# Optimization experiments

Measured on AMD Instinct MI355X. Metric: run time of the kernel, lower is better.

## Reference

```python
import jax, jax.numpy as jnp
import numpy as np

N = 50000      # nodes
E = 800000     # edges
D = 128        # input_dim = nb_hidden = emb_dim
A = 4          # nb_edge_types (edge attr dim)
H = 2          # heads (MyGATConv default)
G = 128        # number of graphs (g.batch)
NEG = 0.2      # leaky_relu negative slope
L = 3          # nb_layers


def _glorot(key, shape):
    lim = np.sqrt(6.0 / (shape[-2] + shape[-1]))
    return jax.random.uniform(key, shape, minval=-lim, maxval=lim, dtype=jnp.float32)


def setup_inputs():
    key = jax.random.key(0)
    ks = jax.random.split(key, 20)
    inp = {
        "x": jax.random.normal(ks[0], (N, D), jnp.float32),
        "edge_index": jax.random.randint(ks[1], (2, E), 0, N, dtype=jnp.int32),
        "edge_attr": jax.random.normal(ks[2], (E, A), jnp.float32),
        "batch": jnp.sort(jax.random.randint(ks[3], (N,), 0, G, dtype=jnp.int32)),
    }
    for l in range(L):
        inp[f"linN{l}"] = _glorot(ks[4 + 4 * l], (D, H * D))
        inp[f"linE{l}"] = _glorot(ks[5 + 4 * l], (A, H * A))
        inp[f"att{l}"] = _glorot(ks[6 + 4 * l], (1, H, 2 * D + A))
        inp[f"bias{l}"] = jnp.zeros((H * D,), jnp.float32)
    inp["fw"] = _glorot(ks[16], (D, 1))
    inp["fb"] = jnp.zeros((1,), jnp.float32)
    return inp


def _gat_layer(x_in, e_in, src, dst, linN, linE, att, bias):
    n = x_in.shape[0]
    x = (x_in @ linN + bias).reshape(n, H, D)              # [N,H,D]
    e = (e_in @ linE).reshape(-1, H, A)                    # [E,H,A]
    # alpha = (cat([x_i, x_j, e], -1) * att).sum(-1); x_i = x[src], x_j = x[dst]
    ai = jnp.einsum('nhc,hc->nh', x, att[0, :, :D])        # per-node, gathered at src
    aj = jnp.einsum('nhc,hc->nh', x, att[0, :, D:2 * D])   # per-node, gathered at dst
    ae = jnp.einsum('ehc,hc->eh', e, att[0, :, 2 * D:])
    alpha = jax.nn.leaky_relu(ai[src] + aj[dst] + ae, NEG)  # [E,H]
    # segment softmax over targets (edge_index[1])
    amax = jax.ops.segment_max(alpha, dst, num_segments=n)
    ex = jnp.exp(alpha - amax[dst])
    denom = jax.ops.segment_sum(ex, dst, num_segments=n)
    alpha = ex / denom[dst]
    # PyG propagate: message = alpha * x[src], scatter-add at dst
    msg = alpha[:, :, None] * x[src]                       # [E,H,D]
    out = jax.ops.segment_sum(msg, dst, num_segments=n) + x
    # concat=False -> mean over heads, then ReLU
    return jax.nn.relu(out.mean(axis=1)), jax.nn.relu(e.mean(axis=1))


def reference(x, edge_index, edge_attr, batch,
              linN0, linE0, att0, bias0,
              linN1, linE1, att1, bias1,
              linN2, linE2, att2, bias2,
              fw, fb):
    src, dst = edge_index[0], edge_index[1]
    params = [(linN0, linE0, att0, bias0),
              (linN1, linE1, att1, bias1),
              (linN2, linE2, att2, bias2)]
    h, e = x, edge_attr
    for (lN, lE, at, b) in params:
        h, e = _gat_layer(h, e, src, dst, lN, lE, at, b)
    pooled = jax.ops.segment_sum(h, batch, num_segments=G)  # global_add_pool -> [G,D]
    y = (pooled @ fw + fb).squeeze(-1)                      # [G]
    return y
```

## Files before the change

### kernel.cpp

```cpp
#include <hip/hip_runtime.h>
#include <hip/hip_bf16.h>

#define DD 128
#define AA 4
#define HH 2

typedef short short8 __attribute__((ext_vector_type(8)));
typedef float f32x4 __attribute__((ext_vector_type(4)));

__device__ inline unsigned short f2bf(float f) {
    unsigned u = __float_as_uint(f);
    unsigned r = (u + 0x7fffu + ((u >> 16) & 1u)) >> 16;
    return (unsigned short)r;
}
__device__ inline float4 unpack_bf16x4(uint2 v) {
    float4 r;
    r.x = __uint_as_float(v.x << 16);
    r.y = __uint_as_float(v.x & 0xffff0000u);
    r.z = __uint_as_float(v.y << 16);
    r.w = __uint_as_float(v.y & 0xffff0000u);
    return r;
}
__device__ inline uint2 pack_bf16x4(float a, float b, float c, float d) {
    uint2 p;
    p.x = (unsigned)f2bf(a) | ((unsigned)f2bf(b) << 16);
    p.y = (unsigned)f2bf(c) | ((unsigned)f2bf(d) << 16);
    return p;
}


__global__ void rank_kernel(const int* __restrict__ dst, int* __restrict__ cnt,
                            int* __restrict__ rank, int E) {
    int e = blockIdx.x * blockDim.x + threadIdx.x;
    if (e < E) rank[e] = atomicAdd(&cnt[dst[e]], 1);
}

__global__ __launch_bounds__(256) void scan1(const int* __restrict__ cnt,
                                             int* __restrict__ bsum, int N,
                                             float* __restrict__ y,
                                             const float* __restrict__ fb) {
    __shared__ int wsh[4];
    int b = blockIdx.x, t = threadIdx.x;
    int lane = t & 63, w = t >> 6;
    if (b == 0 && t < 128) y[t] = fb[0];
    int base = b * 1024;
    int v = 0;
    #pragma unroll
    for (int i = 0; i < 4; ++i) {
        int idx = base + i * 256 + t;
        v += (idx < N) ? cnt[idx] : 0;
    }
    #pragma unroll
    for (int o = 32; o; o >>= 1) v += __shfl_xor(v, o);
    if (lane == 0) wsh[w] = v;
    __syncthreads();
    if (t == 0) bsum[b] = wsh[0] + wsh[1] + wsh[2] + wsh[3];
}

__global__ __launch_bounds__(64) void scan2(int* __restrict__ bsum, int NB,
                                            int* __restrict__ total) {
    int t = threadIdx.x;
    int v = (t < NB) ? bsum[t] : 0;
    int x = v;
    #pragma unroll
    for (int o = 1; o < 64; o <<= 1) {
        int u = __shfl_up(x, o);
        if (t >= o) x += u;
    }
    if (t < NB) bsum[t] = x - v;
    if (t == 63) *total = x;
}

__global__ __launch_bounds__(256) void scan3(const int* __restrict__ cnt,
                                             const int* __restrict__ bsum,
                                             int* __restrict__ row_off, int N) {
    __shared__ int wtot[4];
    __shared__ int carry;
    int b = blockIdx.x, t = threadIdx.x;
    int lane = t & 63, w = t >> 6;
    if (t == 0) carry = bsum[b];
    __syncthreads();
    int base = b * 1024;
    #pragma unroll
    for (int it = 0; it < 4; ++it) {
        int idx = base + it * 256 + t;
        int v = (idx < N) ? cnt[idx] : 0;
        int x = v;
        #pragma unroll
        for (int o = 1; o < 64; o <<= 1) {
            int u = __shfl_up(x, o);
            if (lane >= o) x += u;
        }
        if (lane == 63) wtot[w] = x;
        __syncthreads();
        int woff = 0;
        for (int i = 0; i < w; ++i) woff += wtot[i];
        int c = carry;
        __syncthreads();
        if (t == 255) carry = c + woff + x;
        int ex = c + woff + x - v;
        if (idx < N) row_off[idx] = ex;
        __syncthreads();
    }
}

__global__ void perm_kernel(const int* __restrict__ dst, const int* __restrict__ rank,
                            const int* __restrict__ row_off, int* __restrict__ perm, int E) {
    int e = blockIdx.x * blockDim.x + threadIdx.x;
    if (e >= E) return;
    perm[row_off[dst[e]] + rank[e]] = e;
}


__device__ inline void edge_stage(const float4& ev, const float* __restrict__ linE,
                                  const float* __restrict__ att, float2& ae, float4& enext) {
    float eh[8];
    #pragma unroll
    for (int c = 0; c < 8; ++c)
        eh[c] = ev.x * linE[c] + ev.y * linE[8 + c] + ev.z * linE[16 + c] + ev.w * linE[24 + c];
    float a0 = 0.f, a1 = 0.f;
    #pragma unroll
    for (int a = 0; a < 4; ++a) {
        a0 += eh[a]     * att[2 * DD + a];
        a1 += eh[4 + a] * att[(2 * DD + AA) + 2 * DD + a];
    }
    ae.x = a0; ae.y = a1;
    enext.x = fmaxf(0.5f * (eh[0] + eh[4]), 0.f);
    enext.y = fmaxf(0.5f * (eh[1] + eh[5]), 0.f);
    enext.z = fmaxf(0.5f * (eh[2] + eh[6]), 0.f);
    enext.w = fmaxf(0.5f * (eh[3] + eh[7]), 0.f);
}

__global__ __launch_bounds__(256) void prep_fused(
        const float* __restrict__ ein, const int* __restrict__ src,
        const int* __restrict__ perm,
        const float* __restrict__ linE0, const float* __restrict__ att0,
        const float* __restrict__ linE1, const float* __restrict__ att1,
        const float* __restrict__ linE2, const float* __restrict__ att2,
        int* __restrict__ csr_src,
        float2* __restrict__ ae0, float2* __restrict__ ae1, float2* __restrict__ ae2,
        int E, int ebE,
        const float* __restrict__ X, uint2* __restrict__ As, int N, int ebA,
        const float* __restrict__ W0, const float* __restrict__ W1,
        const float* __restrict__ W2, unsigned short* __restrict__ Bs) {
    int b = blockIdx.x;
    if (b < ebE) {
        int p = b * 256 + threadIdx.x;
        if (p >= E) return;
        int e = perm[p];
        csr_src[p] = src[e];
        float4 ev = ((const float4*)ein)[e];
        float2 ae; float4 en;
        edge_stage(ev, linE0, att0, ae, en); ae0[p] = ae;
        edge_stage(en, linE1, att1, ae, ev); ae1[p] = ae;
        edge_stage(ev, linE2, att2, ae, en); ae2[p] = ae;
    } else if (b < ebE + ebA) {
        int t = (b - ebE) * 256 + threadIdx.x;
        if (t >= N * 32) return;
        int r = t >> 5, kq4 = t & 31;
        float4 v = ((const float4*)X)[t];
        int g = r >> 4, m = r & 15;
        int ks = kq4 >> 3, q = (kq4 >> 1) & 3;
        int cell = ((g * 4 + ks) * 4 + q) * 16 + m;
        As[cell * 2 + (kq4 & 1)] = pack_bf16x4(v.x, v.y, v.z, v.w);
    } else {
        int t = (b - ebE - ebA) * 256 + threadIdx.x;
        if (t >= 3 * 128 * 64) return;
        int l = t / (128 * 64);
        int r = t - l * (128 * 64);
        const float* W = (l == 0) ? W0 : (l == 1) ? W1 : W2;
        unsigned short* B = Bs + (size_t)l * 128 * 256;
        int k = r >> 6, c4g = r & 63;
        float4 v = ((const float4*)W)[r];
        int ct = c4g >> 2, n0 = (c4g & 3) * 4;
        int ks = k >> 5, q = (k >> 3) & 3, j = k & 7;
        int cellbase = ((ct * 4 + ks) * 4 + q) * 16 + n0;
        B[(cellbase + 0) * 8 + j] = f2bf(v.x);
        B[(cellbase + 1) * 8 + j] = f2bf(v.y);
        B[(cellbase + 2) * 8 + j] = f2bf(v.z);
        B[(cellbase + 3) * 8 + j] = f2bf(v.w);
    }
}


__global__ __launch_bounds__(256) void gemm_mfma(const short8* __restrict__ As,
                                                 const short8* __restrict__ Bs,
                                                 const float* __restrict__ bias,
                                                 const float* __restrict__ att,
                                                 uint2* __restrict__ xhb,
                                                 float* __restrict__ aiaj, int Ngroups) {
    __shared__ __align__(16) unsigned short sh[4][16 * 132];
    int w = threadIdx.x >> 6;
    int flat = blockIdx.x * 4 + w;
    int wid = flat >> 1, half = flat & 1;
    int lane = threadIdx.x & 63;
    if (wid >= Ngroups) return;
    int q = lane >> 4, m = lane & 15;

    const short8* Ag = As + (size_t)wid * 256;
    f32x4 acc[8];
    #pragma unroll
    for (int c8 = 0; c8 < 8; ++c8) acc[c8] = (f32x4){0.f, 0.f, 0.f, 0.f};

    #pragma unroll
    for (int ks = 0; ks < 4; ++ks) {
        short8 a = Ag[ks * 64 + lane];
        #pragma unroll
        for (int c8 = 0; c8 < 8; ++c8) {
            short8 b = Bs[(half * 8 + c8) * 256 + ks * 64 + lane];
            acc[c8] = __builtin_amdgcn_mfma_f32_16x16x32_bf16(a, b, acc[c8], 0, 0, 0);
        }
    }

    const float* atth = att + half * (2 * DD + AA);
    float ai[4] = {}, aj[4] = {};
    #pragma unroll
    for (int c8 = 0; c8 < 8; ++c8) {
        int col = c8 * 16 + m;
        float aS = atth[col];
        float aD = atth[DD + col];
        float bv = bias[(half * 8 + c8) * 16 + m];
        #pragma unroll
        for (int reg = 0; reg < 4; ++reg) {
            float val = acc[c8][reg] + bv;
            sh[w][(q * 4 + reg) * 132 + col] = f2bf(val);
            ai[reg] += val * aS;
            aj[reg] += val * aD;
        }
    }
    #pragma unroll
    for (int o = 1; o < 16; o <<= 1) {
        #pragma unroll
        for (int reg = 0; reg < 4; ++reg) {
            ai[reg] += __shfl_xor(ai[reg], o);
            aj[reg] += __shfl_xor(aj[reg], o);
        }
    }
    if (m == 0) {
        #pragma unroll
        for (int reg = 0; reg < 4; ++reg) {
            int row = wid * 16 + q * 4 + reg;
            aiaj[row * 4 + half] = ai[reg];
            aiaj[row * 4 + 2 + half] = aj[reg];
        }
    }
    #pragma unroll
    for (int r2 = 0; r2 < 8; ++r2) {
        int row = r2 * 2 + (lane >> 5);
        uint2 v = *(const uint2*)&sh[w][row * 132 + (lane & 31) * 4];
        xhb[(size_t)(wid * 16 + row) * 64 + half * 32 + (lane & 31)] = v;
    }
}


__global__ __launch_bounds__(256) void aggregate(const uint2* __restrict__ xhb,
                                                 const float* __restrict__ aiaj,
                                                 const float2* __restrict__ ae,
                                                 const int* __restrict__ row_off,
                                                 const int* __restrict__ csr_src,
                                                 uint2* __restrict__ hshuf,
                                                 const float* __restrict__ fw,
                                                 float* __restrict__ pdots, int N) {
    int w = threadIdx.x >> 6;
    int d = blockIdx.x * 4 + w;
    int lane = threadIdx.x & 63;
    if (d >= N) return;
    int s0 = row_off[d], s1 = row_off[d + 1];
    int deg = s1 - s0;
    const float2* aiaj2 = (const float2*)aiaj;
    float2 ajv = aiaj2[d * 2 + 1];

    __shared__ float lex[4][64][2];
    __shared__ int lsrc[4][64];
    float4 acc = {0.f, 0.f, 0.f, 0.f};
    float den0 = 0.f, den1 = 0.f;
    int head = lane >> 5;

    for (int c = 0; c < deg; c += 64) {
        int n = min(64, deg - c);
        if (lane < n) {
            int p = s0 + c + lane;
            int s = csr_src[p];
            float2 aiv = aiaj2[s * 2];
            float2 aev = ae[p];
            float a0 = aiv.x + ajv.x + aev.x; a0 = a0 > 0.f ? a0 : 0.2f * a0;
            float a1 = aiv.y + ajv.y + aev.y; a1 = a1 > 0.f ? a1 : 0.2f * a1;
            float e0 = __expf(a0), e1 = __expf(a1);
            den0 += e0; den1 += e1;
            lex[w][lane][0] = e0; lex[w][lane][1] = e1;
            lsrc[w][lane] = s;
        }
        #pragma unroll 8
        for (int j = 0; j < n; ++j) {
            float wgt = lex[w][j][head];
            float4 xv = unpack_bf16x4(xhb[(size_t)lsrc[w][j] * 64 + lane]);
            acc.x += wgt * xv.x; acc.y += wgt * xv.y;
            acc.z += wgt * xv.z; acc.w += wgt * xv.w;
        }
    }

    #pragma unroll
    for (int o = 32; o; o >>= 1) {
        den0 += __shfl_xor(den0, o);
        den1 += __shfl_xor(den1, o);
    }
    float den = head ? den1 : den0;
    if (deg == 0) den = 1.0f;
    float inv = 1.0f / den;

    float4 xd = unpack_bf16x4(xhb[(size_t)d * 64 + lane]);
    float4 v;
    v.x = acc.x * inv + xd.x;
    v.y = acc.y * inv + xd.y;
    v.z = acc.z * inv + xd.z;
    v.w = acc.w * inv + xd.w;
    float4 o2;
    o2.x = __shfl_xor(v.x, 32);
    o2.y = __shfl_xor(v.y, 32);
    o2.z = __shfl_xor(v.z, 32);
    o2.w = __shfl_xor(v.w, 32);
    if (lane < 32) {
        float4 r;
        r.x = fmaxf(0.5f * (v.x + o2.x), 0.f);
        r.y = fmaxf(0.5f * (v.y + o2.y), 0.f);
        r.z = fmaxf(0.5f * (v.z + o2.z), 0.f);
        r.w = fmaxf(0.5f * (v.w + o2.w), 0.f);
        if (hshuf) {
            int g = d >> 4, m = d & 15;
            int ks = lane >> 3, q = (lane >> 1) & 3;
            int cell = ((g * 4 + ks) * 4 + q) * 16 + m;
            hshuf[cell * 2 + (lane & 1)] = pack_bf16x4(r.x, r.y, r.z, r.w);
        }
        if (pdots) {
            float4 wv = ((const float4*)fw)[lane];
            float pd = r.x * wv.x + r.y * wv.y + r.z * wv.z + r.w * wv.w;
            #pragma unroll
            for (int o = 16; o; o >>= 1) pd += __shfl_xor(pd, o);
            if (lane == 0) pdots[d] = pd;
        }
    }
}


__global__ __launch_bounds__(256) void segpool_kernel(const float* __restrict__ p,
                                                      const int* __restrict__ batch,
                                                      float* __restrict__ y, int N, int G) {
    __shared__ float bins[128];
    int t = threadIdx.x;
    if (t < G) bins[t] = 0.f;
    __syncthreads();
    int per = (N + gridDim.x - 1) / gridDim.x;
    int lo = blockIdx.x * per;
    int hi = min(lo + per, N);
    float acc = 0.f;
    int key = -1;
    for (int i = lo + t; i < hi; i += 256) {
        int k = batch[i];
        float v = p[i];
        if (k != key) {
            if (key >= 0) atomicAdd(&bins[key], acc);
            key = k;
            acc = 0.f;
        }
        acc += v;
    }
    if (key >= 0) atomicAdd(&bins[key], acc);
    __syncthreads();
    if (t < G && bins[t] != 0.f) atomicAdd(&y[t], bins[t]);
}


extern "C" void kernel_launch(void* const* d_in, const int* in_sizes, int n_in,
                              void* d_out, int out_size, void* d_ws, size_t ws_size,
                              hipStream_t stream) {
    const float* x     = (const float*)d_in[0];
    const int*   ei    = (const int*)d_in[1];
    const float* eattr = (const float*)d_in[2];
    const int*   batch = (const int*)d_in[3];
    const float* fw    = (const float*)d_in[16];
    const float* fb    = (const float*)d_in[17];
    float* y = (float*)d_out;

    const int N = in_sizes[0] / DD;
    const int E = in_sizes[1] / 2;
    const int G = out_size;

    const int* src = ei;
    const int* dst = ei + E;

    char* ws = (char*)d_ws;
    size_t off = 0;
    auto carve = [&](size_t bytes) {
        char* p = ws + off;
        off += (bytes + 255) & ~(size_t)255;
        return p;
    };
    uint2*  xhb     = (uint2*)carve((size_t)N * 256 * 2);
    uint2*  S0      = (uint2*)carve((size_t)N * 128 * 2);
    uint2*  S1      = (uint2*)carve((size_t)N * 128 * 2);
    unsigned short* Bs = (unsigned short*)carve((size_t)3 * 128 * 256 * 2);
    float2* ae0     = (float2*)carve((size_t)E * 2 * 4);
    float2* ae1     = (float2*)carve((size_t)E * 2 * 4);
    float2* ae2     = (float2*)carve((size_t)E * 2 * 4);
    float*  aiaj    = (float*)carve((size_t)N * 4 * 4);
    int*    row_off = (int*)carve((size_t)(N + 1) * 4);
    int*    cnt     = (int*)carve((size_t)N * 4);
    int*    rank    = (int*)carve((size_t)E * 4);
    int*    csr_src = (int*)carve((size_t)E * 4);
    int*    perm    = (int*)carve((size_t)E * 4);
    float*  pdots   = (float*)carve((size_t)N * 4);
    int*    bsum    = (int*)carve((size_t)256 * 4);

    const int NB = (N + 1023) / 1024;
    const int Ngroups = N / 16;
    const int eb = (E + 255) / 256;

    hipMemsetAsync(cnt, 0, (size_t)N * 4, stream);
    rank_kernel<<<eb, 256, 0, stream>>>(dst, cnt, rank, E);
    scan1<<<NB, 256, 0, stream>>>(cnt, bsum, N, y, fb);
    scan2<<<1, 64, 0, stream>>>(bsum, NB, row_off + N);
    scan3<<<NB, 256, 0, stream>>>(cnt, bsum, row_off, N);
    perm_kernel<<<eb, 256, 0, stream>>>(dst, rank, row_off, perm, E);

    const int ebA = (N * 32 + 255) / 256;
    const int ebW = (3 * 128 * 64 + 255) / 256;
    prep_fused<<<eb + ebA + ebW, 256, 0, stream>>>(
        eattr, src, perm,
        (const float*)d_in[5], (const float*)d_in[6],
        (const float*)d_in[9], (const float*)d_in[10],
        (const float*)d_in[13], (const float*)d_in[14],
        csr_src, ae0, ae1, ae2, E, eb,
        x, S0, N, ebA,
        (const float*)d_in[4], (const float*)d_in[8], (const float*)d_in[12], Bs);

    int gemm_blocks = (Ngroups * 2 + 3) / 4;
    int agg_blocks = (N + 3) / 4;
    float2* aes[3] = {ae0, ae1, ae2};
    uint2* Ain[3]  = {S0, S1, S0};
    uint2* Aout[3] = {S1, S0, nullptr};

    for (int l = 0; l < 3; ++l) {
        const float* att  = (const float*)d_in[6 + 4 * l];
        const float* bias = (const float*)d_in[7 + 4 * l];
        const short8* Bl  = (const short8*)(Bs + (size_t)l * 128 * 256);

        gemm_mfma<<<gemm_blocks, 256, 0, stream>>>((const short8*)Ain[l], Bl,
                                                   bias, att, xhb, aiaj, Ngroups);
        aggregate<<<agg_blocks, 256, 0, stream>>>(xhb, aiaj, aes[l], row_off, csr_src,
                                                  Aout[l], fw, (l == 2) ? pdots : nullptr, N);
    }

    segpool_kernel<<<128, 256, 0, stream>>>(pdots, batch, y, N, G);
}
```

Measured before the change: 441.7 us.

## Merge scan2 into scan3, store perm and src together, hoist self-feature load

The single-block scan2 kernel is removed. Each scan3 block now rescans the block sums itself, and block 0 writes the total edge count as row_off[N]. perm_kernel writes an int2 pair (edge id, src) in CSR order, so prep_fused no longer does a dependent gather of src[perm[p]] or writes a separate csr_src array. The trade-off is that aggregate now reads 8-byte entries instead of 4-byte csr_src in each of the three layers, and the self-feature load in aggregate is moved earlier so its latency overlaps with the edge loop.

```diff
diff --git a/kernel.cpp b/kernel.cpp
--- a/kernel.cpp
+++ b/kernel.cpp
@@ -57,28 +57,26 @@
     if (t == 0) bsum[b] = wsh[0] + wsh[1] + wsh[2] + wsh[3];
 }
 
-__global__ __launch_bounds__(64) void scan2(int* __restrict__ bsum, int NB,
-                                            int* __restrict__ total) {
-    int t = threadIdx.x;
-    int v = (t < NB) ? bsum[t] : 0;
-    int x = v;
-    #pragma unroll
-    for (int o = 1; o < 64; o <<= 1) {
-        int u = __shfl_up(x, o);
-        if (t >= o) x += u;
-    }
-    if (t < NB) bsum[t] = x - v;
-    if (t == 63) *total = x;
-}
-
 __global__ __launch_bounds__(256) void scan3(const int* __restrict__ cnt,
                                              const int* __restrict__ bsum,
-                                             int* __restrict__ row_off, int N) {
+                                             int* __restrict__ row_off,
+                                             int N, int NB, int E) {
     __shared__ int wtot[4];
     __shared__ int carry;
     int b = blockIdx.x, t = threadIdx.x;
     int lane = t & 63, w = t >> 6;
-    if (t == 0) carry = bsum[b];
+    if (w == 0) {
+        int v = (lane < NB) ? bsum[lane] : 0;
+        int x = v;
+        #pragma unroll
+        for (int o = 1; o < 64; o <<= 1) {
+            int u = __shfl_up(x, o);
+            if (lane >= o) x += u;
+        }
+        int base = (b == 0) ? 0 : __shfl(x, b - 1);
+        if (lane == 0) carry = base;
+    }
+    if (b == 0 && t == 0) row_off[N] = E;
     __syncthreads();
     int base = b * 1024;
     #pragma unroll
@@ -104,11 +102,14 @@
     }
 }
 
-__global__ void perm_kernel(const int* __restrict__ dst, const int* __restrict__ rank,
-                            const int* __restrict__ row_off, int* __restrict__ perm, int E) {
+__global__ void perm_kernel(const int* __restrict__ src, const int* __restrict__ dst,
+                            const int* __restrict__ rank,
+                            const int* __restrict__ row_off,
+                            int2* __restrict__ perm2, int E) {
     int e = blockIdx.x * blockDim.x + threadIdx.x;
     if (e >= E) return;
-    perm[row_off[dst[e]] + rank[e]] = e;
+    int2 v; v.x = e; v.y = src[e];
+    perm2[row_off[dst[e]] + rank[e]] = v;
 }
 
 
@@ -132,12 +133,10 @@
 }
 
 __global__ __launch_bounds__(256) void prep_fused(
-        const float* __restrict__ ein, const int* __restrict__ src,
-        const int* __restrict__ perm,
+        const float* __restrict__ ein, const int2* __restrict__ perm2,
         const float* __restrict__ linE0, const float* __restrict__ att0,
         const float* __restrict__ linE1, const float* __restrict__ att1,
         const float* __restrict__ linE2, const float* __restrict__ att2,
-        int* __restrict__ csr_src,
         float2* __restrict__ ae0, float2* __restrict__ ae1, float2* __restrict__ ae2,
         int E, int ebE,
         const float* __restrict__ X, uint2* __restrict__ As, int N, int ebA,
@@ -147,8 +146,7 @@
     if (b < ebE) {
         int p = b * 256 + threadIdx.x;
         if (p >= E) return;
-        int e = perm[p];
-        csr_src[p] = src[e];
+        int e = perm2[p].x;
         float4 ev = ((const float4*)ein)[e];
         float2 ae; float4 en;
         edge_stage(ev, linE0, att0, ae, en); ae0[p] = ae;
@@ -257,7 +255,7 @@
                                                  const float* __restrict__ aiaj,
                                                  const float2* __restrict__ ae,
                                                  const int* __restrict__ row_off,
-                                                 const int* __restrict__ csr_src,
+                                                 const int2* __restrict__ perm2,
                                                  uint2* __restrict__ hshuf,
                                                  const float* __restrict__ fw,
                                                  float* __restrict__ pdots, int N) {
@@ -269,6 +267,7 @@
     int deg = s1 - s0;
     const float2* aiaj2 = (const float2*)aiaj;
     float2 ajv = aiaj2[d * 2 + 1];
+    float4 xd = unpack_bf16x4(xhb[(size_t)d * 64 + lane]);
 
     __shared__ float lex[4][64][2];
     __shared__ int lsrc[4][64];
@@ -280,7 +279,7 @@
         int n = min(64, deg - c);
         if (lane < n) {
             int p = s0 + c + lane;
-            int s = csr_src[p];
+            int s = perm2[p].y;
             float2 aiv = aiaj2[s * 2];
             float2 aev = ae[p];
             float a0 = aiv.x + ajv.x + aev.x; a0 = a0 > 0.f ? a0 : 0.2f * a0;
@@ -308,7 +307,6 @@
     if (deg == 0) den = 1.0f;
     float inv = 1.0f / den;
 
-    float4 xd = unpack_bf16x4(xhb[(size_t)d * 64 + lane]);
     float4 v;
     v.x = acc.x * inv + xd.x;
     v.y = acc.y * inv + xd.y;
@@ -406,8 +404,7 @@
     int*    row_off = (int*)carve((size_t)(N + 1) * 4);
     int*    cnt     = (int*)carve((size_t)N * 4);
     int*    rank    = (int*)carve((size_t)E * 4);
-    int*    csr_src = (int*)carve((size_t)E * 4);
-    int*    perm    = (int*)carve((size_t)E * 4);
+    int2*   perm2   = (int2*)carve((size_t)E * 8);
     float*  pdots   = (float*)carve((size_t)N * 4);
     int*    bsum    = (int*)carve((size_t)256 * 4);
 
@@ -418,18 +415,17 @@
     hipMemsetAsync(cnt, 0, (size_t)N * 4, stream);
     rank_kernel<<<eb, 256, 0, stream>>>(dst, cnt, rank, E);
     scan1<<<NB, 256, 0, stream>>>(cnt, bsum, N, y, fb);
-    scan2<<<1, 64, 0, stream>>>(bsum, NB, row_off + N);
-    scan3<<<NB, 256, 0, stream>>>(cnt, bsum, row_off, N);
-    perm_kernel<<<eb, 256, 0, stream>>>(dst, rank, row_off, perm, E);
+    scan3<<<NB, 256, 0, stream>>>(cnt, bsum, row_off, N, NB, E);
+    perm_kernel<<<eb, 256, 0, stream>>>(src, dst, rank, row_off, perm2, E);
 
     const int ebA = (N * 32 + 255) / 256;
     const int ebW = (3 * 128 * 64 + 255) / 256;
     prep_fused<<<eb + ebA + ebW, 256, 0, stream>>>(
-        eattr, src, perm,
+        eattr, perm2,
         (const float*)d_in[5], (const float*)d_in[6],
         (const float*)d_in[9], (const float*)d_in[10],
         (const float*)d_in[13], (const float*)d_in[14],
-        csr_src, ae0, ae1, ae2, E, eb,
+        ae0, ae1, ae2, E, eb,
         x, S0, N, ebA,
         (const float*)d_in[4], (const float*)d_in[8], (const float*)d_in[12], Bs);
 
@@ -446,7 +442,7 @@
 
         gemm_mfma<<<gemm_blocks, 256, 0, stream>>>((const short8*)Ain[l], Bl,
                                                    bias, att, xhb, aiaj, Ngroups);
-        aggregate<<<agg_blocks, 256, 0, stream>>>(xhb, aiaj, aes[l], row_off, csr_src,
+        aggregate<<<agg_blocks, 256, 0, stream>>>(xhb, aiaj, aes[l], row_off, perm2,
                                                   Aout[l], fw, (l == 2) ? pdots : nullptr, N);
     }
 
```

Result: no change. 433.6 us (-1.9%).
